# Kernel optimization log

Hardware: AMD Instinct MI355X
Metric: run time of the kernel (lower is better)

## Reference

```python
import math
import jax, jax.numpy as jnp
import numpy as np

SIGMA_S = 2.0
SIGMA_R = 0.1
KERNEL_SIZE = 9
PAD = KERNEL_SIZE // 2
_COORDS = list(range(-PAD, PAD + 1))
OFFSETS = [(i, j) for i in _COORDS for j in _COORDS]
SPATIAL_W = [math.exp(-((i * i + j * j) / (2.0 * SIGMA_S ** 2))) for i, j in OFFSETS]

B, C, H, W = 16, 1, 768, 1024


def setup_inputs() -> dict:
    key = jax.random.key(0)
    k1, k2, k3 = jax.random.split(key, 3)
    depth = jax.random.uniform(k1, (B, C, H, W), dtype=jnp.float32)
    vals = jax.random.uniform(k2, (B, C, H, W), dtype=jnp.float32)
    mask = jax.random.uniform(k3, (B, C, H, W)) < 0.05
    sparse = jnp.where(mask, vals, jnp.float32(1.0))
    return {"sparse": sparse, "depth": depth}


def reference(sparse, depth):
    pad = PAD
    # sparse padded with the 'missing' sentinel 1.0; depth reflect-padded
    sp = jnp.pad(sparse, ((0, 0), (0, 0), (pad, pad), (pad, pad)), mode="constant", constant_values=1.0)
    dp = jnp.pad(depth, ((0, 0), (0, 0), (pad, pad), (pad, pad)), mode="reflect")
    num = jnp.zeros_like(sparse)
    den = jnp.zeros_like(sparse)
    inv_two_sr2 = 1.0 / (2.0 * SIGMA_R ** 2)
    Hh, Ww = sparse.shape[-2], sparse.shape[-1]
    for (dy, dx), w in zip(OFFSETS, SPATIAL_W):
        sp_shift = sp[..., pad + dy : pad + dy + Hh, pad + dx : pad + dx + Ww]
        dp_shift = dp[..., pad + dy : pad + dy + Hh, pad + dx : pad + dx + Ww]
        valid = (sp_shift != 1.0).astype(sparse.dtype)
        diff = dp_shift - depth
        range_w = jnp.exp(-(diff * diff) * inv_two_sr2)
        w_total = w * range_w * valid
        num = num + w_total * sp_shift
        den = den + w_total
    out = num / (den + 1e-8)
    out = jnp.where(den < 1e-8, jnp.ones_like(out), out)
    return out
```

## Files before the change

kernel.cpp:

```cpp
#include <hip/hip_runtime.h>


#define HH 768
#define WW 1024
#define BB 16
#define CS (-0.18033688011112042f)
#define CR (-72.13475204444817f)

#define TS 68
#define TROWS 31
#define TSIZE (TROWS * TS)
#define TF4   (TSIZE / 4)

typedef float f2 __attribute__((ext_vector_type(2)));

__device__ __forceinline__ int rfl(int x) { return __builtin_amdgcn_readfirstlane(x); }
__device__ __forceinline__ float rlanef(float v, int b) {
    return __int_as_float(__builtin_amdgcn_readlane(__float_as_int(v), b));
}
__device__ __forceinline__ f2 splat(float x) { f2 r; r.x = x; r.y = x; return r; }

__global__ __launch_bounds__(256) void jbf_kernel(
    const float* __restrict__ sparse,
    const float* __restrict__ depth,
    float* __restrict__ out)
{
    __shared__ __align__(16) float Tab[TSIZE];
    const int tid  = (int)threadIdx.x;
    const int lane = tid & 63;
    const int wv   = tid >> 6;

    {
        float4 s; s.x = -1e30f; s.y = -1e30f; s.z = -1e30f; s.w = -1e30f;
        float4* t4 = (float4*)Tab;
        #pragma unroll
        for (int i = 0; i < 3; ++i) {
            const int idx = tid + 256 * i;
            if (idx < TF4) t4[idx] = s;
        }
    }
    __syncthreads();
    if (tid < 81) {
        const int rr = (tid * 57) >> 9;
        const int cc = tid - 9 * rr;
        const float dy = (float)(rr - 4), dx = (float)(cc - 4);
        Tab[(rr + 11) * TS + cc + 19] = CS * fmaf(dy, dy, dx * dx);
    }
    __syncthreads();

    const int ty  = rfl(((int)blockIdx.y << 4) + ((wv >> 1) << 3));
    const int py0 = rfl(min(max(ty - 4, 0), HH - 16));
    const int tyoff = ty - py0;
    const int sbrow = TS * (15 - tyoff);

    const size_t plane = (size_t)blockIdx.z * (size_t)(HH * WW);
    const float* sp = sparse + plane;
    const float* dp = depth  + plane;

    const int r  = lane >> 2;
    const int c0 = (lane & 3) << 1;
    const int my = lane >> 3, mx = lane & 7;
    const int gy = ty + my;
    const int clane_w = my * TS + mx;
    const f2 crp = splat(CR);

    const int txb = rfl((int)blockIdx.x * 128 + ((wv & 1) << 4));

#define STAGE(TX, PX0, S0, S1, S2, D0, D1, D2, M0, M1)                    \
    const int PX0 = rfl(min(max((TX) - 4, 0), WW - 24));                  \
    {                                                                      \
        const float* wbs = sp + (size_t)(py0 + r) * WW + PX0 + c0;        \
        const float* wbd = dp + (size_t)(py0 + r) * WW + PX0 + c0;        \
        S0 = *(const f2*)(wbs);                                            \
        S1 = *(const f2*)(wbs + 8);                                        \
        S2 = *(const f2*)(wbs + 16);                                       \
        D0 = *(const f2*)(wbd);                                            \
        D1 = *(const f2*)(wbd + 8);                                        \
        D2 = *(const f2*)(wbd + 16);                                       \
        M0 = dp[(size_t)gy * WW + (TX) + mx];                              \
        M1 = dp[(size_t)gy * WW + (TX) + mx + 8];                          \
    }

#define PROCESS(TX, PX0, S0, S1, S2, D0, D1, D2, M0, M1)                  \
    {                                                                      \
        const int txoff = (TX) - PX0;                            \
        const int sbase0 = sbrow + (23 - txoff) - 8;                       \
        f2 nmyd; nmyd.x = -(M0); nmyd.y = -(M1);                           \
        f2 numA = splat(0.0f), denA = splat(0.0f);                         \
        f2 numB = splat(0.0f), denB = splat(0.0f);                         \
        _Pragma("unroll")                                                  \
        for (int j = 0; j < 3; ++j) {                                      \
            const f2 s2 = (j == 0) ? S0 : (j == 1) ? S1 : S2;              \
            const f2 d2 = (j == 0) ? D0 : (j == 1) ? D1 : D2;              \
            _Pragma("unroll")                                              \
            for (int k = 0; k < 2; ++k) {                                  \
                const float svk = k ? s2.y : s2.x;                         \
                const float dvk = k ? d2.y : d2.x;                         \
                const int sbase = sbase0 + 8 * j + k;            \
                unsigned long long m = __ballot(svk != 1.0f);              \
                while (m) {                                   \
                    const int b0 = (int)__builtin_ctzll(m);                \
                    m &= (m - 1ull);                                       \
                    {                                                      \
                        const float sv_e = rlanef(svk, b0);                \
                        const float dv_e = rlanef(dvk, b0);                \
                        const int SW = sbase + (b0 >> 2) * TS              \
                                       + ((b0 & 3) << 1);        \
                        const float* tb = Tab + (SW - clane_w);            \
                        f2 tp; tp.x = tb[8]; tp.y = tb[0];   \
                        const f2 diff = nmyd + splat(dv_e);                \
                        const f2 q = diff * crp;                           \
                        const f2 arg = q * diff + tp;          \
                        f2 w; w.x = __builtin_amdgcn_exp2f(arg.x);         \
                        w.y = __builtin_amdgcn_exp2f(arg.y);               \
                        denA += w;                                         \
                        numA += w * splat(sv_e);               \
                    }                                                      \
                    if (m) {                                  \
                        const int b1 = (int)__builtin_ctzll(m);            \
                        m &= (m - 1ull);                                   \
                        const float sv_e = rlanef(svk, b1);                \
                        const float dv_e = rlanef(dvk, b1);                \
                        const int SW = sbase + (b1 >> 2) * TS              \
                                       + ((b1 & 3) << 1);                  \
                        const float* tb = Tab + (SW - clane_w);            \
                        f2 tp; tp.x = tb[8]; tp.y = tb[0];                 \
                        const f2 diff = nmyd + splat(dv_e);                \
                        const f2 q = diff * crp;                           \
                        const f2 arg = q * diff + tp;                      \
                        f2 w; w.x = __builtin_amdgcn_exp2f(arg.x);         \
                        w.y = __builtin_amdgcn_exp2f(arg.y);               \
                        denB += w;                                         \
                        numB += w * splat(sv_e);                           \
                    }                                                      \
                }                                                          \
            }                                                              \
        }                                                                  \
        const float n0 = numA.x + numB.x, n1 = numA.y + numB.y;            \
        const float e0 = denA.x + denB.x, e1 = denA.y + denB.y;            \
        float r0 = n0 * __builtin_amdgcn_rcpf(e0 + 1e-8f);                 \
        r0 = (e0 < 1e-8f) ? 1.0f : r0;                                     \
        float r1 = n1 * __builtin_amdgcn_rcpf(e1 + 1e-8f);                 \
        r1 = (e1 < 1e-8f) ? 1.0f : r1;                                     \
        float* op = out + plane + (size_t)gy * WW + (TX) + mx;             \
        op[0] = r0;                                                        \
        op[8] = r1;                                                        \
    }

    f2 sA0, sA1, sA2, dA0, dA1, dA2; float mA0, mA1;
    f2 sB0, sB1, sB2, dB0, dB1, dB2; float mB0, mB1;

    const int tx0 = txb;
    const int tx1 = txb + 32;
    const int tx2 = txb + 64;
    const int tx3 = txb + 96;

    STAGE(tx0, px0a, sA0, sA1, sA2, dA0, dA1, dA2, mA0, mA1)
    STAGE(tx1, px0b, sB0, sB1, sB2, dB0, dB1, dB2, mB0, mB1)
    PROCESS(tx0, px0a, sA0, sA1, sA2, dA0, dA1, dA2, mA0, mA1)
    STAGE(tx2, px0c, sA0, sA1, sA2, dA0, dA1, dA2, mA0, mA1)
    PROCESS(tx1, px0b, sB0, sB1, sB2, dB0, dB1, dB2, mB0, mB1)
    STAGE(tx3, px0d, sB0, sB1, sB2, dB0, dB1, dB2, mB0, mB1)
    PROCESS(tx2, px0c, sA0, sA1, sA2, dA0, dA1, dA2, mA0, mA1)
    PROCESS(tx3, px0d, sB0, sB1, sB2, dB0, dB1, dB2, mB0, mB1)

#undef STAGE
#undef PROCESS
}

extern "C" void kernel_launch(void* const* d_in, const int* in_sizes, int n_in,
                              void* d_out, int out_size, void* d_ws, size_t ws_size,
                              hipStream_t stream)
{
    const float* sparse = (const float*)d_in[0];
    const float* depth  = (const float*)d_in[1];
    float* out = (float*)d_out;
    dim3 grid(WW / 128, HH / 16, BB);
    jbf_kernel<<<grid, dim3(256, 1, 1), 0, stream>>>(sparse, depth, out);
}
```

Before: 175.5 us.

## Compact valid sparse samples into per-wave LDS list before weighting

Instead of iterating the ballot mask with ctz and readlane for each valid sample, each wave writes valid (value, depth, table offset) entries into a per-wave LDS buffer using mbcnt prefix positions. It then loops over the compacted list two entries at a time, reading entries via LDS broadcast loads, and pads with sentinel entries that point at a -1e30 table slot so they contribute zero. This removes the serial scalar mask walking and readlane dependencies from the inner loop. In exchange it adds LDS writes, extra shared memory (which may lower occupancy), and a fallback path for overflow beyond the buffer capacity.

```diff
diff --git a/kernel.cpp b/kernel.cpp
--- a/kernel.cpp
+++ b/kernel.cpp
@@ -11,6 +11,9 @@
 #define TROWS 31
 #define TSIZE (TROWS * TS)
 #define TF4   (TSIZE / 4)
+#define CAP   128
+#define SENT_B 2400
+#define LDSF (TSIZE + 4 * (CAP + 2) * 4)
 
 typedef float f2 __attribute__((ext_vector_type(2)));
 
@@ -25,10 +28,12 @@
     const float* __restrict__ depth,
     float* __restrict__ out)
 {
-    __shared__ __align__(16) float Tab[TSIZE];
+    __shared__ __align__(16) float Lds[LDSF];
+    float* Tab = Lds;
     const int tid  = (int)threadIdx.x;
     const int lane = tid & 63;
     const int wv   = tid >> 6;
+    float4* ebuf = (float4*)(Lds + TSIZE) + wv * (CAP + 2);
 
     {
         float4 s; s.x = -1e30f; s.y = -1e30f; s.z = -1e30f; s.w = -1e30f;
@@ -62,6 +67,7 @@
     const int my = lane >> 3, mx = lane & 7;
     const int gy = ty + my;
     const int clane_w = my * TS + mx;
+    const int lwr = (lane >> 2) * TS + ((lane & 3) << 1);
     const f2 crp = splat(CR);
 
     const int txb = rfl((int)blockIdx.x * 128 + ((wv & 1) << 4));
@@ -84,10 +90,11 @@
 #define PROCESS(TX, PX0, S0, S1, S2, D0, D1, D2, M0, M1)                  \
     {                                                                      \
         const int txoff = (TX) - PX0;                            \
-        const int sbase0 = sbrow + (23 - txoff) - 8;                       \
+        const int sb0 = sbrow + (23 - txoff) - 8;                \
         f2 nmyd; nmyd.x = -(M0); nmyd.y = -(M1);                           \
         f2 numA = splat(0.0f), denA = splat(0.0f);                         \
         f2 numB = splat(0.0f), denB = splat(0.0f);                         \
+        int base = 0;                                                      \
         _Pragma("unroll")                                                  \
         for (int j = 0; j < 3; ++j) {                                      \
             const f2 s2 = (j == 0) ? S0 : (j == 1) ? S1 : S2;              \
@@ -96,52 +103,79 @@
             for (int k = 0; k < 2; ++k) {                                  \
                 const float svk = k ? s2.y : s2.x;                         \
                 const float dvk = k ? d2.y : d2.x;                         \
-                const int sbase = sbase0 + 8 * j + k;            \
-                unsigned long long m = __ballot(svk != 1.0f);              \
-                while (m) {                                   \
-                    const int b0 = (int)__builtin_ctzll(m);                \
-                    m &= (m - 1ull);                                       \
-                    {                                                      \
-                        const float sv_e = rlanef(svk, b0);                \
-                        const float dv_e = rlanef(dvk, b0);                \
-                        const int SW = sbase + (b0 >> 2) * TS              \
-                                       + ((b0 & 3) << 1);        \
-                        const float* tb = Tab + (SW - clane_w);            \
-                        f2 tp; tp.x = tb[8]; tp.y = tb[0];   \
-                        const f2 diff = nmyd + splat(dv_e);                \
-                        const f2 q = diff * crp;                           \
-                        const f2 arg = q * diff + tp;          \
-                        f2 w; w.x = __builtin_amdgcn_exp2f(arg.x);         \
-                        w.y = __builtin_amdgcn_exp2f(arg.y);               \
-                        denA += w;                                         \
-                        numA += w * splat(sv_e);               \
-                    }                                                      \
-                    if (m) {                                  \
-                        const int b1 = (int)__builtin_ctzll(m);            \
-                        m &= (m - 1ull);                                   \
-                        const float sv_e = rlanef(svk, b1);                \
-                        const float dv_e = rlanef(dvk, b1);                \
-                        const int SW = sbase + (b1 >> 2) * TS              \
-                                       + ((b1 & 3) << 1);                  \
-                        const float* tb = Tab + (SW - clane_w);            \
-                        f2 tp; tp.x = tb[8]; tp.y = tb[0];                 \
-                        const f2 diff = nmyd + splat(dv_e);                \
-                        const f2 q = diff * crp;                           \
-                        const f2 arg = q * diff + tp;                      \
-                        f2 w; w.x = __builtin_amdgcn_exp2f(arg.x);         \
-                        w.y = __builtin_amdgcn_exp2f(arg.y);               \
-                        denB += w;                                         \
-                        numB += w * splat(sv_e);                           \
-                    }                                                      \
+                const bool p = (svk != 1.0f);                              \
+                unsigned long long m = __ballot(p);                        \
+                const int swb = (sb0 + 8 * j + k + lwr) << 2;              \
+                const int pre = (int)__builtin_amdgcn_mbcnt_hi(            \
+                    (unsigned)(m >> 32),                                   \
+                    __builtin_amdgcn_mbcnt_lo((unsigned)m, 0u));           \
+                const int wpos = base + pre;                               \
+                if (p && wpos < CAP) {                                     \
+                    float4 e; e.x = svk; e.y = dvk;                        \
+                    e.z = __int_as_float(swb); e.w = 0.f;                  \
+                    ebuf[wpos] = e;                                        \
+                }                                                          \
+                unsigned long long of = __ballot(p && wpos >= CAP);        \
+                base += __builtin_popcountll(m);                           \
+                while (of) {                             \
+                    const int b0 = (int)__builtin_ctzll(of);               \
+                    of &= (of - 1ull);                                     \
+                    const float sv_e = rlanef(svk, b0);                    \
+                    const float dv_e = rlanef(dvk, b0);                    \
+                    const int SW = (sb0 + 8 * j + k) + (b0 >> 2) * TS      \
+                                   + ((b0 & 3) << 1);                      \
+                    const float* tb = Tab + (SW - clane_w);                \
+                    f2 tp; tp.x = tb[8]; tp.y = tb[0];                     \
+                    const f2 diff = nmyd + splat(dv_e);                    \
+                    const f2 q = diff * crp;                               \
+                    const f2 arg = q * diff + tp;                          \
+                    f2 w; w.x = __builtin_amdgcn_exp2f(arg.x);             \
+                    w.y = __builtin_amdgcn_exp2f(arg.y);                   \
+                    denA += w;                                             \
+                    numA += w * splat(sv_e);                               \
                 }                                                          \
             }                                                              \
         }                                                                  \
+        const int n = min(base, CAP);                                      \
+        if (lane < 2) {                             \
+            float4 e; e.x = 1.0f; e.y = 0.f;                               \
+            e.z = __int_as_float(SENT_B); e.w = 0.f;                       \
+            ebuf[n + lane] = e;                                            \
+        }                                                                  \
+        for (int i = 0; i < n; i += 2) {             \
+            const float4 e0 = ebuf[i];                 \
+            const float4 e1 = ebuf[i + 1];                                 \
+            const float* tb0 = (const float*)((const char*)Tab             \
+                               + __float_as_int(e0.z)) - clane_w;          \
+            const float* tb1 = (const float*)((const char*)Tab             \
+                               + __float_as_int(e1.z)) - clane_w;          \
+            f2 tp0; tp0.x = tb0[8]; tp0.y = tb0[0];                        \
+            f2 tp1; tp1.x = tb1[8]; tp1.y = tb1[0];                        \
+            {                                                              \
+                const f2 diff = nmyd + splat(e0.y);                        \
+                const f2 q = diff * crp;                                   \
+                const f2 arg = q * diff + tp0;                             \
+                f2 w; w.x = __builtin_amdgcn_exp2f(arg.x);                 \
+                w.y = __builtin_amdgcn_exp2f(arg.y);                       \
+                denA += w;                                                 \
+                numA += w * splat(e0.x);                                   \
+            }                                                              \
+            {                                                              \
+                const f2 diff = nmyd + splat(e1.y);                        \
+                const f2 q = diff * crp;                                   \
+                const f2 arg = q * diff + tp1;                             \
+                f2 w; w.x = __builtin_amdgcn_exp2f(arg.x);                 \
+                w.y = __builtin_amdgcn_exp2f(arg.y);                       \
+                denB += w;                                                 \
+                numB += w * splat(e1.x);                                   \
+            }                                                              \
+        }                                                                  \
         const float n0 = numA.x + numB.x, n1 = numA.y + numB.y;            \
-        const float e0 = denA.x + denB.x, e1 = denA.y + denB.y;            \
-        float r0 = n0 * __builtin_amdgcn_rcpf(e0 + 1e-8f);                 \
-        r0 = (e0 < 1e-8f) ? 1.0f : r0;                                     \
-        float r1 = n1 * __builtin_amdgcn_rcpf(e1 + 1e-8f);                 \
-        r1 = (e1 < 1e-8f) ? 1.0f : r1;                                     \
+        const float e0s = denA.x + denB.x, e1s = denA.y + denB.y;          \
+        float r0 = n0 * __builtin_amdgcn_rcpf(e0s + 1e-8f);                \
+        r0 = (e0s < 1e-8f) ? 1.0f : r0;                                    \
+        float r1 = n1 * __builtin_amdgcn_rcpf(e1s + 1e-8f);                \
+        r1 = (e1s < 1e-8f) ? 1.0f : r1;                                    \
         float* op = out + plane + (size_t)gy * WW + (TX) + mx;             \
         op[0] = r0;                                                        \
         op[8] = r1;                                                        \
```

New measurement: 175.0 us. Within noise of the previous version (-0.3%).
